# Kernel optimization log

Hardware: AMD Instinct MI355X
Metric: run time of the kernel (lower is better)

## Reference

```python
import jax, jax.numpy as jnp
import numpy as np

B, T, C, H, K = 4, 2048, 1024, 16, 64
CHUNK = 64
NUM_LAYERS, LAYER_ID = 12, 6
D_MIX, D_DECAY = 32, 64


def setup_inputs() -> dict:
    key = jax.random.key(0)
    ks = jax.random.split(key, 12)
    x = jax.random.normal(ks[0], (B, T, C), jnp.float32)
    shift_state_in = jax.random.normal(ks[1], (B, C), jnp.float32)
    wkv_state_in = jnp.zeros((B, H, K, K), jnp.float32)

    r01 = LAYER_ID / max(NUM_LAYERS - 1, 1)
    r10 = 1.0 - LAYER_ID / NUM_LAYERS
    ddd = (np.arange(C, dtype=np.float64) / C)
    maa = lambda p: jnp.asarray((1.0 - ddd ** p).reshape(1, 1, C), jnp.float32)
    time_maa_x = maa(r10)
    time_maa_w = maa(r10)
    time_maa_k = maa(r10)
    time_maa_v = jnp.asarray((1.0 - (ddd ** r10 + 0.3 * r01)).reshape(1, 1, C), jnp.float32)
    time_maa_r = maa(0.5 * r10)
    time_maa_g = maa(0.5 * r10)
    time_maa_w1 = jax.random.uniform(ks[2], (C, D_MIX * 5), jnp.float32, -0.01, 0.01)
    time_maa_w2 = jax.random.uniform(ks[3], (5, D_MIX, C), jnp.float32, -0.01, 0.01)

    n = np.arange(C, dtype=np.float64)
    time_decay = jnp.asarray((-6 + 5 * (n / (C - 1)) ** (0.7 + 1.3 * r01)).reshape(1, 1, C), jnp.float32)
    time_decay_w1 = jax.random.uniform(ks[4], (C, D_DECAY), jnp.float32, -0.01, 0.01)
    time_decay_w2 = jax.random.uniform(ks[5], (D_DECAY, C), jnp.float32, -0.01, 0.01)

    zig = ((n + 1) % 3 - 1) * 0.1
    time_faaaa = jnp.asarray((r01 * (1 - n / (C - 1)) + zig).reshape(H, K), jnp.float32)
    lucid_temperature = jnp.ones((1, H, 1, 1), jnp.float32)

    s = 0.02
    W_r = jax.random.normal(ks[6], (C, C), jnp.float32) * s
    W_k = jax.random.normal(ks[7], (C, C), jnp.float32) * s
    W_v = jax.random.normal(ks[8], (C, C), jnp.float32) * s
    W_g = jax.random.normal(ks[9], (C, C), jnp.float32) * s
    W_o = jax.random.normal(ks[10], (C, C), jnp.float32) * s
    ln_gamma = jnp.ones((C,), jnp.float32)
    ln_beta = jnp.zeros((C,), jnp.float32)

    return dict(x=x, shift_state_in=shift_state_in, wkv_state_in=wkv_state_in,
                time_maa_x=time_maa_x, time_maa_w=time_maa_w, time_maa_k=time_maa_k,
                time_maa_v=time_maa_v, time_maa_r=time_maa_r, time_maa_g=time_maa_g,
                time_maa_w1=time_maa_w1, time_maa_w2=time_maa_w2,
                time_decay=time_decay, time_decay_w1=time_decay_w1, time_decay_w2=time_decay_w2,
                time_faaaa=time_faaaa, lucid_temperature=lucid_temperature,
                W_r=W_r, W_k=W_k, W_v=W_v, W_g=W_g, W_o=W_o,
                ln_gamma=ln_gamma, ln_beta=ln_beta)


def _forward(x, shift_state_in, wkv_state_in, time_maa_x, time_maa_w, time_maa_k,
             time_maa_v, time_maa_r, time_maa_g, time_maa_w1, time_maa_w2,
             time_decay, time_decay_w1, time_decay_w2, time_faaaa, lucid_temperature,
             W_r, W_k, W_v, W_g, W_o, ln_gamma, ln_beta):
    # ddlerp token shift
    dxprev = jnp.concatenate([shift_state_in[:, None, :], x[:, :-1]], axis=1) - x
    xxx = jnp.tanh((x + dxprev * time_maa_x) @ time_maa_w1).reshape(B, T, 5, D_MIX)
    m = jnp.einsum('btfd,fdc->fbtc', xxx, time_maa_w2)  # (5,B,T,C)
    mw, mk, mv, mr, mg = m[0], m[1], m[2], m[3], m[4]
    xw = x + dxprev * (time_maa_w + mw)
    xk = x + dxprev * (time_maa_k + mk)
    xv = x + dxprev * (time_maa_v + mv)
    xr = x + dxprev * (time_maa_r + mr)
    xg = x + dxprev * (time_maa_g + mg)

    r = xr @ W_r.T
    k = xk @ W_k.T
    v = xv @ W_v.T
    g = jax.nn.silu(xg @ W_g.T)
    w = time_decay + jnp.tanh(xw @ time_decay_w1) @ time_decay_w2

    tohead = lambda a: a.reshape(B, T, H, K).transpose(0, 2, 1, 3)  # (B,H,T,K)
    r_h, k_h, v_h = tohead(r), tohead(k), tohead(v)
    w_h = -jnp.exp(tohead(w))  # log-decay, negative
    u = time_faaaa.reshape(1, H, 1, K)
    temp = jax.nn.softplus(lucid_temperature)  # (1,H,1,1)

    n_chunks = T // CHUNK
    tochunks = lambda a: a.reshape(B, H, n_chunks, CHUNK, K).transpose(2, 0, 1, 3, 4)
    eye = jnp.eye(CHUNK, dtype=jnp.float32)
    mid = CHUNK // 2

    def step(state, inp):
        r_c, k_c, v_c, w_log = inp  # each (B,H,cs,K)
        w_cum = jnp.cumsum(w_log, axis=-2)
        w_shift = jnp.pad(w_cum[..., :-1, :], ((0, 0), (0, 0), (1, 0), (0, 0)))
        offset = w_shift[..., mid:mid + 1, :]
        r_decay = jnp.exp(jnp.clip(w_shift - offset, -30, 30))
        k_inv_decay = jnp.exp(jnp.clip(offset - w_cum, -30, 30))
        A = jnp.einsum('bhtk,bhsk->bhts', r_c * r_decay, k_c * k_inv_decay)
        A = jnp.tril(A, -1) + eye * jnp.sum(r_c * (u * k_c), axis=-1)[..., None]
        k_norm = k_c / jnp.maximum(jnp.linalg.norm(k_c, axis=-1, keepdims=True), 1e-12)
        K_gram = jnp.einsum('bhtk,bhsk->bhts', k_norm, k_norm)
        P = eye + jnp.exp(jnp.clip(temp * K_gram, -20, 20))
        P_v = jnp.linalg.solve(P, v_c)
        w_intra = jnp.exp(jnp.clip(w_cum - w_log, -30, 30))
        y = A @ P_v + (r_c * w_intra) @ state
        w_sum = jnp.sum(w_log, axis=-2, keepdims=True)  # (B,H,1,K)
        w_inter = jnp.exp(jnp.clip(w_sum - w_cum, -30, 30))
        new_state = state * jnp.exp(w_sum) + jnp.einsum('bhtk,bhtv->bhkv', k_c * w_inter, v_c)
        return new_state, y

    state_out, ys = jax.lax.scan(
        step, wkv_state_in,
        (tochunks(r_h), tochunks(k_h), tochunks(v_h), tochunks(w_h)))
    # (n,B,H,cs,K) -> (B,T,C)
    y = ys.transpose(1, 2, 0, 3, 4).reshape(B, H, T, K).transpose(0, 2, 1, 3).reshape(B, T, C)

    # GroupNorm with n_head groups, eps = 1e-5 * head_size_divisor**2
    eps = 1e-5 * 64.0
    yg = y.reshape(B, T, H, K)
    mu = yg.mean(axis=-1, keepdims=True)
    var = yg.var(axis=-1, keepdims=True)
    yn = (yg - mu) / jnp.sqrt(var + eps)
    yn = yn * ln_gamma.reshape(1, 1, H, K) + ln_beta.reshape(1, 1, H, K)
    yn = yn.reshape(B, T, C)

    out = (yn * g) @ W_o.T
    return out, x[:, -1], state_out


def reference(x, shift_state_in, wkv_state_in, time_maa_x, time_maa_w, time_maa_k,
              time_maa_v, time_maa_r, time_maa_g, time_maa_w1, time_maa_w2,
              time_decay, time_decay_w1, time_decay_w2, time_faaaa, lucid_temperature,
              W_r, W_k, W_v, W_g, W_o, ln_gamma, ln_beta):
    return _forward(x, shift_state_in, wkv_state_in, time_maa_x, time_maa_w, time_maa_k,
                    time_maa_v, time_maa_r, time_maa_g, time_maa_w1, time_maa_w2,
                    time_decay, time_decay_w1, time_decay_w2, time_faaaa, lucid_temperature,
                    W_r, W_k, W_v, W_g, W_o, ln_gamma, ln_beta)
```

## Files before the change

kernel.cpp:

```cpp
#include <hip/hip_runtime.h>
#include <cstdint>
#include <cstddef>

typedef unsigned short ushort_t;
#define DEVI __device__ __forceinline__

constexpr int Bc = 4, Tc = 2048, Cc = 1024, Hc = 16;
constexpr int BT = Bc * Tc;
constexpr int NCHUNK = Tc / 64;

using f32x4  = __attribute__((ext_vector_type(4))) float;
using bf16x8 = __attribute__((ext_vector_type(8))) __bf16;

DEVI ushort_t f2bf(float f) {
  union { float f; unsigned u; } v; v.f = f;
  unsigned r = v.u + 0x7fffu + ((v.u >> 16) & 1u);
  return (ushort_t)(r >> 16);
}
DEVI float bf2f(ushort_t u) {
  union { unsigned u; float f; } v; v.u = ((unsigned)u) << 16; return v.f;
}
DEVI float clip30(float x) { return fminf(fmaxf(x, -30.f), 30.f); }
DEVI float clip20(float x) { return fminf(fmaxf(x, -20.f), 20.f); }

DEVI float4 bf4up(uint2 r) {
  float4 v;
  v.x = bf2f((ushort_t)(r.x & 0xffff)); v.y = bf2f((ushort_t)(r.x >> 16));
  v.z = bf2f((ushort_t)(r.y & 0xffff)); v.w = bf2f((ushort_t)(r.y >> 16));
  return v;
}
DEVI uint2 f4pk(float4 v) {
  uint2 r;
  r.x = (unsigned)f2bf(v.x) | ((unsigned)f2bf(v.y) << 16);
  r.y = (unsigned)f2bf(v.z) | ((unsigned)f2bf(v.w) << 16);
  return r;
}

DEVI void gload_lds16(const ushort_t* g, ushort_t* l) {
  __builtin_amdgcn_global_load_lds(
      (const __attribute__((address_space(1))) void*)g,
      (__attribute__((address_space(3))) void*)l, 16, 0, 0);
}

#define GETEL(V4, E) ((E) == 0 ? (V4).x : (E) == 1 ? (V4).y : (E) == 2 ? (V4).z : (V4).w)
#define SETEL(V4, E, VAL) do { if ((E) == 0) (V4).x = (VAL); else if ((E) == 1) (V4).y = (VAL); \
                               else if ((E) == 2) (V4).z = (VAL); else (V4).w = (VAL); } while (0)

__global__ void k_f2bf5(const float* __restrict__ i0, const float* __restrict__ i1,
                        const float* __restrict__ i2, const float* __restrict__ i3,
                        const float* __restrict__ i4,
                        ushort_t* __restrict__ o0, ushort_t* __restrict__ o1,
                        ushort_t* __restrict__ o2, ushort_t* __restrict__ o3,
                        ushort_t* __restrict__ o4) {
  int z = blockIdx.z;
  const float* in = (z == 0) ? i0 : (z == 1) ? i1 : (z == 2) ? i2 : (z == 3) ? i3 : i4;
  ushort_t* out   = (z == 0) ? o0 : (z == 1) ? o1 : (z == 2) ? o2 : (z == 3) ? o3 : o4;
  int i = blockIdx.x * 256 + threadIdx.x;
  if (i < Cc * Cc / 4) {
    float4 v = *(const float4*)(in + (size_t)i * 4);
    ushort4 o;
    o.x = f2bf(v.x); o.y = f2bf(v.y); o.z = f2bf(v.z); o.w = f2bf(v.w);
    *(ushort4*)(out + (size_t)i * 4) = o;
  }
}

__global__ void k_prep(const float* __restrict__ w2, const float* __restrict__ w1,
                       const float* __restrict__ dw1, const float* __restrict__ x,
                       ushort_t* __restrict__ w2t, ushort_t* __restrict__ w1t,
                       ushort_t* __restrict__ dw1t, float* __restrict__ xlast) {
  int i = blockIdx.x * 256 + threadIdx.x;
  if (i < 163840) {
    int c = i / 160, fd = i % 160;
    w2t[i] = f2bf(w2[(size_t)fd * 1024 + c]);
  } else if (i < 327680) {
    int j = i - 163840; int n = j >> 10, r = j & 1023;
    w1t[j] = f2bf(w1[(size_t)r * 160 + n]);
  } else if (i < 393216) {
    int j = i - 327680; int n = j >> 10, r = j & 1023;
    dw1t[j] = f2bf(dw1[(size_t)r * 64 + n]);
  } else if (i < 397312) {
    int j = i - 393216; int b = j >> 10, c = j & 1023;
    xlast[j] = x[((size_t)b * Tc + Tc - 1) * Cc + c];
  }
}

__global__ __launch_bounds__(256) void k_shift_tanh(
    const float* __restrict__ x, const float* __restrict__ sst,
    const float* __restrict__ tmx, const ushort_t* __restrict__ Wt,
    ushort_t* __restrict__ outv) {
  constexpr int NCOLS = 160, NF = NCOLS / 16;
  int tid = threadIdx.x;
  int wave = tid >> 6, lane = tid & 63;
  int row0 = (blockIdx.x * 4 + wave) * 16;
  int lr = lane & 15, lk = (lane >> 4) * 8;
  int rg = row0 + lr;
  int tt = rg & (Tc - 1);
  const float* xrow = x + (size_t)rg * Cc;
  const float* prow = (tt == 0) ? (sst + (size_t)(rg >> 11) * Cc) : (xrow - Cc);
  f32x4 acc[NF];
  #pragma unroll
  for (int n = 0; n < NF; ++n) acc[n] = (f32x4){0.f, 0.f, 0.f, 0.f};
  for (int k0 = 0; k0 < 1024; k0 += 32) {
    int c0 = k0 + lk;
    float4 xa = *(const float4*)(xrow + c0), xb = *(const float4*)(xrow + c0 + 4);
    float4 pa = *(const float4*)(prow + c0), pb = *(const float4*)(prow + c0 + 4);
    float4 ta = *(const float4*)(tmx + c0), tb = *(const float4*)(tmx + c0 + 4);
    union { bf16x8 v; uint2 u[2]; } cv;
    cv.u[0] = f4pk(make_float4(xa.x + (pa.x - xa.x) * ta.x, xa.y + (pa.y - xa.y) * ta.y,
                               xa.z + (pa.z - xa.z) * ta.z, xa.w + (pa.w - xa.w) * ta.w));
    cv.u[1] = f4pk(make_float4(xb.x + (pb.x - xb.x) * tb.x, xb.y + (pb.y - xb.y) * tb.y,
                               xb.z + (pb.z - xb.z) * tb.z, xb.w + (pb.w - xb.w) * tb.w));
    #pragma unroll
    for (int n = 0; n < NF; ++n) {
      bf16x8 b = *(const bf16x8*)&Wt[(size_t)(n * 16 + lr) * 1024 + k0 + lk];
      acc[n] = __builtin_amdgcn_mfma_f32_16x16x32_bf16(cv.v, b, acc[n], 0, 0, 0);
    }
  }
  #pragma unroll
  for (int n = 0; n < NF; ++n) {
    #pragma unroll
    for (int q = 0; q < 4; ++q) {
      int row = row0 + (lane >> 4) * 4 + q;
      size_t oi = (size_t)row * NCOLS + n * 16 + lr;
      outv[oi] = f2bf(tanhf(acc[n][q]));
    }
  }
}

template<int NCOLS, int OBF>
__global__ __launch_bounds__(256) void k_tanh_mfma(const ushort_t* __restrict__ A,
                                                   const ushort_t* __restrict__ Wt,
                                                   void* __restrict__ outv) {
  constexpr int NF = NCOLS / 16;
  int tid = threadIdx.x;
  int wave = tid >> 6, lane = tid & 63;
  int row0 = (blockIdx.x * 4 + wave) * 16;
  int lr = lane & 15, lk = (lane >> 4) * 8;
  f32x4 acc[NF];
  #pragma unroll
  for (int n = 0; n < NF; ++n) acc[n] = (f32x4){0.f, 0.f, 0.f, 0.f};
  for (int k0 = 0; k0 < 1024; k0 += 32) {
    bf16x8 a = *(const bf16x8*)&A[(size_t)(row0 + lr) * 1024 + k0 + lk];
    #pragma unroll
    for (int n = 0; n < NF; ++n) {
      bf16x8 b = *(const bf16x8*)&Wt[(size_t)(n * 16 + lr) * 1024 + k0 + lk];
      acc[n] = __builtin_amdgcn_mfma_f32_16x16x32_bf16(a, b, acc[n], 0, 0, 0);
    }
  }
  #pragma unroll
  for (int n = 0; n < NF; ++n) {
    #pragma unroll
    for (int q = 0; q < 4; ++q) {
      int row = row0 + (lane >> 4) * 4 + q;
      size_t oi = (size_t)row * NCOLS + n * 16 + lr;
      float v = tanhf(acc[n][q]);
      if (OBF == 1) ((ushort_t*)outv)[oi] = f2bf(v);
      else          ((float*)outv)[oi] = v;
    }
  }
}

__global__ __launch_bounds__(256) void k_mix5m(
    const float* __restrict__ x, const float* __restrict__ sst,
    const ushort_t* __restrict__ t160b, const ushort_t* __restrict__ w2t,
    const float* __restrict__ maaw, const float* __restrict__ maak,
    const float* __restrict__ maav, const float* __restrict__ maar,
    const float* __restrict__ maag,
    ushort_t* __restrict__ xw, ushort_t* __restrict__ xk, ushort_t* __restrict__ xv,
    ushort_t* __restrict__ xr, ushort_t* __restrict__ xg) {
  __shared__ __align__(16) ushort_t smem[23040];
  ushort_t* As = smem;
  ushort_t* Bs = smem + 64 * 168;
  ushort_t* sT = smem;
  int tid = threadIdx.x;
  int lane = tid & 63;
  int bRow = blockIdx.x * 64, bCol = blockIdx.y * 64;
  #pragma unroll
  for (int i = 0; i < 5; ++i) {
    int e = tid + i * 256;
    int r = e / 20, cc = (e % 20) * 8;
    *(int4*)&As[r * 168 + cc] = *(const int4*)&t160b[(size_t)(bRow + r) * 160 + cc];
    *(int4*)&Bs[r * 168 + cc] = *(const int4*)&w2t[(size_t)(bCol + r) * 160 + cc];
  }
  __syncthreads();
  int wm = tid >> 7, wn = (tid >> 6) & 1;
  f32x4 acc[5][2][2];
  #pragma unroll
  for (int f = 0; f < 5; ++f)
    #pragma unroll
    for (int m = 0; m < 2; ++m)
      #pragma unroll
      for (int n = 0; n < 2; ++n) acc[f][m][n] = (f32x4){0.f, 0.f, 0.f, 0.f};
  #pragma unroll
  for (int f = 0; f < 5; ++f) {
    bf16x8 af[2], bfv[2];
    #pragma unroll
    for (int m = 0; m < 2; ++m)
      af[m] = *(const bf16x8*)&As[(wm * 32 + m * 16 + (lane & 15)) * 168 + f * 32 + (lane >> 4) * 8];
    #pragma unroll
    for (int n = 0; n < 2; ++n)
      bfv[n] = *(const bf16x8*)&Bs[(wn * 32 + n * 16 + (lane & 15)) * 168 + f * 32 + (lane >> 4) * 8];
    #pragma unroll
    for (int m = 0; m < 2; ++m)
      #pragma unroll
      for (int n = 0; n < 2; ++n)
        acc[f][m][n] = __builtin_amdgcn_mfma_f32_16x16x32_bf16(af[m], bfv[n], acc[f][m][n], 0, 0, 0);
  }
  __syncthreads();
  #pragma unroll
  for (int n = 0; n < 2; ++n) {
    int colL = wn * 32 + n * 16 + (lane & 15);
    int col = bCol + colL;
    float mw_c = maaw[col], mk_c = maak[col], mv_c = maav[col];
    float mr_c = maar[col], mg_c = maag[col];
    #pragma unroll
    for (int m = 0; m < 2; ++m) {
      int rowL0 = wm * 32 + m * 16 + (lane >> 4) * 4;
      #pragma unroll
      for (int q = 0; q < 4; ++q) {
        int rL = rowL0 + q;
        int rg = bRow + rL;
        int tt = rg & (Tc - 1);
        size_t g = (size_t)rg * Cc + col;
        float xv0 = x[g];
        float xprev = (tt == 0) ? sst[(size_t)(rg >> 11) * Cc + col] : x[g - Cc];
        float dv = xprev - xv0;
        sT[0 * 4608 + rL * 72 + colL] = f2bf(xv0 + dv * (mw_c + acc[0][m][n][q]));
        sT[1 * 4608 + rL * 72 + colL] = f2bf(xv0 + dv * (mk_c + acc[1][m][n][q]));
        sT[2 * 4608 + rL * 72 + colL] = f2bf(xv0 + dv * (mv_c + acc[2][m][n][q]));
        sT[3 * 4608 + rL * 72 + colL] = f2bf(xv0 + dv * (mr_c + acc[3][m][n][q]));
        sT[4 * 4608 + rL * 72 + colL] = f2bf(xv0 + dv * (mg_c + acc[4][m][n][q]));
      }
    }
  }
  __syncthreads();
  #pragma unroll
  for (int f = 0; f < 5; ++f) {
    ushort_t* dst = (f == 0) ? xw : (f == 1) ? xk : (f == 2) ? xv : (f == 3) ? xr : xg;
    #pragma unroll
    for (int j = 0; j < 2; ++j) {
      int e = tid + j * 256;
      int r = e >> 3, ch = (e & 7) * 8;
      *(int4*)&dst[(size_t)(bRow + r) * 1024 + bCol + ch] =
          *(const int4*)&sT[f * 4608 + r * 72 + ch];
    }
  }
}

template<int EPI, int OBF>
DEVI void gemm_body(const ushort_t* __restrict__ A, const ushort_t* __restrict__ Wt,
                    void* __restrict__ outv, ushort_t* As, ushort_t* Bs,
                    int bRow, int bCol) {
  int tid = threadIdx.x;
  int wave = tid >> 6, lane = tid & 63;
  int wm = wave >> 1, wn = wave & 1;
  int lr = lane >> 2;
  int lkb = (((lane & 3) ^ ((lane >> 3) & 3))) * 8;
  int pch = ((lane >> 4) ^ ((lane >> 1) & 3)) * 8;
  f32x4 zero4 = {0.f, 0.f, 0.f, 0.f};
  f32x4 acc[4][4];
  #pragma unroll
  for (int m = 0; m < 4; ++m)
    #pragma unroll
    for (int n = 0; n < 4; ++n) acc[m][n] = zero4;

#define STAGEK(OFS, K0) do { \
    _Pragma("unroll") \
    for (int i = 0; i < 2; ++i) { \
      int row = (wave + 4 * i) * 16 + lr; \
      gload_lds16(A + (size_t)(bRow + row) * 1024 + (K0) + lkb, &As[(OFS) + (wave + 4 * i) * 512]); \
      gload_lds16(Wt + (size_t)(bCol + row) * 1024 + (K0) + lkb, &Bs[(OFS) + (wave + 4 * i) * 512]); \
    } } while (0)
#define CMP(OFS) do { \
    bf16x8 af[4], bfv[4]; \
    _Pragma("unroll") \
    for (int m = 0; m < 4; ++m) \
      af[m] = *(const bf16x8*)&As[(OFS) + (wm * 64 + m * 16 + (lane & 15)) * 32 + pch]; \
    _Pragma("unroll") \
    for (int n = 0; n < 4; ++n) \
      bfv[n] = *(const bf16x8*)&Bs[(OFS) + (wn * 64 + n * 16 + (lane & 15)) * 32 + pch]; \
    _Pragma("unroll") \
    for (int m = 0; m < 4; ++m) \
      _Pragma("unroll") \
      for (int n = 0; n < 4; ++n) \
        acc[m][n] = __builtin_amdgcn_mfma_f32_16x16x32_bf16(af[m], bfv[n], acc[m][n], 0, 0, 0); \
  } while (0)

  for (int k0 = 0; k0 < 1024; k0 += 64) {
    STAGEK(0, k0);
    STAGEK(4096, k0 + 32);
    __syncthreads();
    CMP(0);
    CMP(4096);
    __syncthreads();
  }
#undef STAGEK
#undef CMP

  #pragma unroll
  for (int m = 0; m < 4; ++m) {
    int row = bRow + wm * 64 + m * 16 + (lane >> 4) * 4;
    #pragma unroll
    for (int n = 0; n < 4; ++n) {
      int col = bCol + wn * 64 + n * 16 + (lane & 15);
      #pragma unroll
      for (int q = 0; q < 4; ++q) {
        float v = acc[m][n][q];
        if (EPI == 1) v = v / (1.f + __expf(-v));
        size_t oi = (size_t)(row + q) * 1024 + col;
        if (OBF == 1) ((ushort_t*)outv)[oi] = f2bf(v);
        else          ((float*)outv)[oi] = v;
      }
    }
  }
}

__global__ __launch_bounds__(256) void k_gemm4(
    const ushort_t* __restrict__ A0, const ushort_t* __restrict__ A1,
    const ushort_t* __restrict__ A2, const ushort_t* __restrict__ A3,
    const ushort_t* __restrict__ W0, const ushort_t* __restrict__ W1,
    const ushort_t* __restrict__ W2, const ushort_t* __restrict__ W3,
    ushort_t* __restrict__ O0, ushort_t* __restrict__ O1,
    ushort_t* __restrict__ O2, ushort_t* __restrict__ O3) {
  __shared__ __align__(16) ushort_t As[2 * 128 * 32];
  __shared__ __align__(16) ushort_t Bs[2 * 128 * 32];
  int z = blockIdx.z;
  const ushort_t* A  = (z == 0) ? A0 : (z == 1) ? A1 : (z == 2) ? A2 : A3;
  const ushort_t* Wt = (z == 0) ? W0 : (z == 1) ? W1 : (z == 2) ? W2 : W3;
  ushort_t* out      = (z == 0) ? O0 : (z == 1) ? O1 : (z == 2) ? O2 : O3;
  if (z == 3) gemm_body<1, 1>(A, Wt, out, As, Bs, blockIdx.x * 128, blockIdx.y * 128);
  else        gemm_body<0, 1>(A, Wt, out, As, Bs, blockIdx.x * 128, blockIdx.y * 128);
}

__global__ __launch_bounds__(256) void k_gemm_bm64(const ushort_t* __restrict__ A,
                                                   const ushort_t* __restrict__ Wt,
                                                   float* __restrict__ out) {
  __shared__ __align__(16) ushort_t As[2 * 64 * 32];
  __shared__ __align__(16) ushort_t Bs[2 * 128 * 32];
  int tid = threadIdx.x;
  int wave = tid >> 6, lane = tid & 63;
  int lr = lane >> 2;
  int lkb = (((lane & 3) ^ ((lane >> 3) & 3))) * 8;
  int pch = ((lane >> 4) ^ ((lane >> 1) & 3)) * 8;
  int bRow = blockIdx.x * 64, bCol = blockIdx.y * 128;
  f32x4 acc[4][2];
  #pragma unroll
  for (int m = 0; m < 4; ++m)
    #pragma unroll
    for (int n = 0; n < 2; ++n) acc[m][n] = (f32x4){0.f, 0.f, 0.f, 0.f};

#define STAGEK64(OA, OB, K0) do { \
    { int row = wave * 16 + lr; \
      gload_lds16(A + (size_t)(bRow + row) * 1024 + (K0) + lkb, &As[(OA) + wave * 512]); } \
    _Pragma("unroll") \
    for (int i = 0; i < 2; ++i) { \
      int row = (wave + 4 * i) * 16 + lr; \
      gload_lds16(Wt + (size_t)(bCol + row) * 1024 + (K0) + lkb, &Bs[(OB) + (wave + 4 * i) * 512]); \
    } } while (0)
#define CMP64(OA, OB) do { \
    bf16x8 af[4], bfv[2]; \
    _Pragma("unroll") \
    for (int m = 0; m < 4; ++m) \
      af[m] = *(const bf16x8*)&As[(OA) + (m * 16 + (lane & 15)) * 32 + pch]; \
    _Pragma("unroll") \
    for (int n = 0; n < 2; ++n) \
      bfv[n] = *(const bf16x8*)&Bs[(OB) + (wave * 32 + n * 16 + (lane & 15)) * 32 + pch]; \
    _Pragma("unroll") \
    for (int m = 0; m < 4; ++m) \
      _Pragma("unroll") \
      for (int n = 0; n < 2; ++n) \
        acc[m][n] = __builtin_amdgcn_mfma_f32_16x16x32_bf16(af[m], bfv[n], acc[m][n], 0, 0, 0); \
  } while (0)

  for (int k0 = 0; k0 < 1024; k0 += 64) {
    STAGEK64(0, 0, k0);
    STAGEK64(2048, 4096, k0 + 32);
    __syncthreads();
    CMP64(0, 0);
    CMP64(2048, 4096);
    __syncthreads();
  }
#undef STAGEK64
#undef CMP64

  #pragma unroll
  for (int m = 0; m < 4; ++m) {
    int row = bRow + m * 16 + (lane >> 4) * 4;
    #pragma unroll
    for (int n = 0; n < 2; ++n) {
      int col = bCol + wave * 32 + n * 16 + (lane & 15);
      #pragma unroll
      for (int q = 0; q < 4; ++q)
        out[(size_t)(row + q) * 1024 + col] = acc[m][n][q];
    }
  }
}

__global__ __launch_bounds__(256) void k_preA(
    const ushort_t* __restrict__ rbuf, const ushort_t* __restrict__ kbuf,
    const ushort_t* __restrict__ vbf,
    const ushort_t* __restrict__ t64bf, const float* __restrict__ dw2,
    const float* __restrict__ tdec, const float* __restrict__ faaaa,
    ushort_t* __restrict__ rwbf, ushort_t* __restrict__ kvbf, ushort_t* __restrict__ knbuf,
    ushort_t* __restrict__ Abf, float* __restrict__ esum) {
  __shared__ __align__(16) char ubuf[16640 + 9216 + 9216];
  float* wc = (float*)ubuf;
  ushort_t* sS = (ushort_t*)ubuf;
  ushort_t* sA = (ushort_t*)(ubuf + 16640);
  ushort_t* sB = (ushort_t*)(ubuf + 16640 + 9216);
  __shared__ float sred[4 * 64];
  __shared__ float sdiag[64];
  __shared__ float snrm[64];
  int bx = blockIdx.x;
  int ci = bx & 31, bh = bx >> 5;
  int b = bh >> 4, h = bh & 15;
  int tid = threadIdx.x;
  int w = tid >> 6, lane = tid & 63;
  int c = lane;
  int row0g = b * Tc + ci * 64;
  size_t base = (size_t)row0g * Cc + (size_t)h * 64;

  #pragma unroll
  for (int j = 0; j < 2; ++j) {
    int e = tid + j * 256; int r = e >> 3, cc = (e & 7) * 8;
    *(int4*)&sA[r * 72 + cc] = *(const int4*)&t64bf[(size_t)(row0g + r) * 64 + cc];
  }
  for (int i = 0; i < 16; ++i) {
    int e = tid + i * 256; int r = e >> 6, cc = e & 63;
    sB[cc * 72 + r] = f2bf(dw2[(size_t)r * Cc + h * 64 + cc]);
  }
  float rv[16], kv[16];
  #pragma unroll
  for (int i = 0; i < 16; ++i) {
    size_t g = base + (size_t)(w * 16 + i) * Cc + c;
    rv[i] = bf2f(rbuf[g]); kv[i] = bf2f(kbuf[g]);
  }
  __syncthreads();
  {
    int rbase = w * 16;
    bf16x8 a0 = *(const bf16x8*)&sA[(rbase + (lane & 15)) * 72 + (lane >> 4) * 8];
    bf16x8 a1 = *(const bf16x8*)&sA[(rbase + (lane & 15)) * 72 + 32 + (lane >> 4) * 8];
    #pragma unroll
    for (int ct = 0; ct < 4; ++ct) {
      bf16x8 b0 = *(const bf16x8*)&sB[(ct * 16 + (lane & 15)) * 72 + (lane >> 4) * 8];
      bf16x8 b1 = *(const bf16x8*)&sB[(ct * 16 + (lane & 15)) * 72 + 32 + (lane >> 4) * 8];
      f32x4 acc = {0.f, 0.f, 0.f, 0.f};
      acc = __builtin_amdgcn_mfma_f32_16x16x32_bf16(a0, b0, acc, 0, 0, 0);
      acc = __builtin_amdgcn_mfma_f32_16x16x32_bf16(a1, b1, acc, 0, 0, 0);
      int s = ct * 16 + (lane & 15);
      #pragma unroll
      for (int q = 0; q < 4; ++q) {
        int t = rbase + (lane >> 4) * 4 + q;
        wc[t * 65 + s] = acc[q];
      }
    }
  }
  __syncthreads();
  float wv[16];
  {
    float td = tdec[h * 64 + c];
    #pragma unroll
    for (int i = 0; i < 16; ++i)
      wv[i] = -__expf(td + wc[(w * 16 + i) * 65 + c]);
  }
  {
    float s = 0.f;
    #pragma unroll
    for (int i = 0; i < 16; ++i) s += wv[i];
    sred[w * 64 + c] = s;
  }
  __syncthreads();
  {
    float run = 0.f;
    for (int ww = 0; ww < w; ++ww) run += sred[ww * 64 + c];
    #pragma unroll
    for (int i = 0; i < 16; ++i) {
      run += wv[i]; wv[i] = run;
      wc[(w * 16 + i) * 65 + c] = run;
    }
    if (w == 3) esum[((size_t)bh * 32 + ci) * 64 + c] = __expf(run);
  }
  {
    float u_c = faaaa[h * 64 + c];
    #pragma unroll
    for (int i = 0; i < 16; ++i) {
      float p = rv[i] * kv[i] * u_c;
      float n2 = kv[i] * kv[i];
      #pragma unroll
      for (int o = 32; o; o >>= 1) { p += __shfl_xor(p, o, 64); n2 += __shfl_xor(n2, o, 64); }
      if (lane == 0) {
        sdiag[w * 16 + i] = p;
        snrm[w * 16 + i] = 1.f / fmaxf(sqrtf(n2), 1e-12f);
      }
    }
  }
  __syncthreads();
  float off32 = wc[31 * 65 + c];
  float wc63 = wc[63 * 65 + c];
  #pragma unroll
  for (int i = 0; i < 16; ++i) {
    int t = w * 16 + i;
    size_t g = base + (size_t)t * Cc + c;
    float wsh = (i == 0) ? ((w == 0) ? 0.f : wc[(t - 1) * 65 + c]) : wv[i - 1];
    rwbf[g] = f2bf(rv[i] * __expf(clip30(wsh)));
    sA[t * 72 + c] = f2bf(rv[i] * __expf(clip30(wsh - off32)));
    sB[t * 72 + c] = f2bf(kv[i] * __expf(clip30(off32 - wv[i])));
    knbuf[g] = f2bf(kv[i] * snrm[t]);
  }
  __syncthreads();
  {
    int rbase = w * 16;
    bf16x8 a0 = *(const bf16x8*)&sA[(rbase + (lane & 15)) * 72 + (lane >> 4) * 8];
    bf16x8 a1 = *(const bf16x8*)&sA[(rbase + (lane & 15)) * 72 + 32 + (lane >> 4) * 8];
    #pragma unroll
    for (int ct = 0; ct < 4; ++ct) {
      bf16x8 b0 = *(const bf16x8*)&sB[(ct * 16 + (lane & 15)) * 72 + (lane >> 4) * 8];
      bf16x8 b1 = *(const bf16x8*)&sB[(ct * 16 + (lane & 15)) * 72 + 32 + (lane >> 4) * 8];
      f32x4 acc = {0.f, 0.f, 0.f, 0.f};
      acc = __builtin_amdgcn_mfma_f32_16x16x32_bf16(a0, b0, acc, 0, 0, 0);
      acc = __builtin_amdgcn_mfma_f32_16x16x32_bf16(a1, b1, acc, 0, 0, 0);
      int s = ct * 16 + (lane & 15);
      #pragma unroll
      for (int q = 0; q < 4; ++q) {
        int t = rbase + (lane >> 4) * 4 + q;
        float val = (t > s) ? acc[q] : ((t == s) ? sdiag[t] : 0.f);
        sS[t * 72 + s] = f2bf(val);
      }
    }
  }
  __syncthreads();
  #pragma unroll
  for (int j = 0; j < 2; ++j) {
    int e = tid + j * 256;
    int r = e >> 3, ch = (e & 7) * 8;
    *(int4*)&Abf[(size_t)bx * 4096 + r * 64 + ch] = *(const int4*)&sS[r * 72 + ch];
  }
  #pragma unroll
  for (int i = 0; i < 16; ++i) {
    int t = w * 16 + i;
    sA[c * 72 + t] = f2bf(kv[i] * __expf(clip30(wc63 - wv[i])));
    sB[c * 72 + t] = vbf[base + (size_t)t * Cc + c];
  }
  __syncthreads();
  {
    int rbase = w * 16;
    bf16x8 a0 = *(const bf16x8*)&sA[(rbase + (lane & 15)) * 72 + (lane >> 4) * 8];
    bf16x8 a1 = *(const bf16x8*)&sA[(rbase + (lane & 15)) * 72 + 32 + (lane >> 4) * 8];
    #pragma unroll
    for (int ct = 0; ct < 4; ++ct) {
      bf16x8 b0 = *(const bf16x8*)&sB[(ct * 16 + (lane & 15)) * 72 + (lane >> 4) * 8];
      bf16x8 b1 = *(const bf16x8*)&sB[(ct * 16 + (lane & 15)) * 72 + 32 + (lane >> 4) * 8];
      f32x4 acc = {0.f, 0.f, 0.f, 0.f};
      acc = __builtin_amdgcn_mfma_f32_16x16x32_bf16(a0, b0, acc, 0, 0, 0);
      acc = __builtin_amdgcn_mfma_f32_16x16x32_bf16(a1, b1, acc, 0, 0, 0);
      int j = ct * 16 + (lane & 15);
      #pragma unroll
      for (int q = 0; q < 4; ++q) {
        int ii = rbase + (lane >> 4) * 4 + q;
        sS[ii * 72 + j] = f2bf(acc[q]);
      }
    }
  }
  __syncthreads();
  #pragma unroll
  for (int j = 0; j < 2; ++j) {
    int e = tid + j * 256;
    int r = e >> 3, ch = (e & 7) * 8;
    *(int4*)&kvbf[base + (size_t)r * Cc + ch] = *(const int4*)&sS[r * 72 + ch];
  }
}

__global__ __launch_bounds__(256) void k_preB(
    const ushort_t* __restrict__ knbuf, const ushort_t* __restrict__ vbf,
    const ushort_t* __restrict__ Abf, const ushort_t* __restrict__ rwbf,
    const ushort_t* __restrict__ statebuf, const float* __restrict__ ltemp,
    const ushort_t* __restrict__ gbuf, const float* __restrict__ gamma,
    const float* __restrict__ beta, ushort_t* __restrict__ ong) {
  __shared__ __align__(16) ushort_t sKX[64 * 72];
  __shared__ __align__(16) ushort_t sAb[64 * 72];
  __shared__ __align__(16) char ubuf[64 * 72 * 2 * 2];
  __shared__ __align__(16) float pivbuf[2][192];
  __shared__ float colbuf[2][64];
  __shared__ float diagbuf[64];
  float* sP = (float*)ubuf;
  ushort_t* sRW = (ushort_t*)ubuf;
  ushort_t* sSTt = (ushort_t*)(ubuf + 64 * 72 * 2);

  int bx = blockIdx.x;
  int ci = bx & 31, bh = bx >> 5;
  int b = bh >> 4, h = bh & 15;
  int tid = threadIdx.x;
  int w = tid >> 6, lane = tid & 63;
  int rg = tid >> 4, cg = tid & 15;
  size_t base = ((size_t)(b * Tc + ci * 64)) * Cc + (size_t)h * 64;

  #pragma unroll
  for (int j = 0; j < 2; ++j) {
    int e = tid + j * 256;
    int r = e >> 3, cc = (e & 7) * 8;
    *(int4*)&sKX[r * 72 + cc] = *(const int4*)&knbuf[base + (size_t)r * Cc + cc];
    *(int4*)&sAb[r * 72 + cc] = *(const int4*)&Abf[(size_t)bx * 4096 + (size_t)r * 64 + cc];
  }
  float4 A0, A1, A2, A3, B0, B1, B2, B3;
  if (cg >= 8) {
#define LDV(R, AR, BR) do { \
      int4 raw = *(const int4*)(vbf + base + (size_t)(4 * rg + (R)) * Cc + (cg - 8) * 8); \
      (AR).x = bf2f((ushort_t)(raw.x & 0xffff)); (AR).y = bf2f((ushort_t)((unsigned)raw.x >> 16)); \
      (AR).z = bf2f((ushort_t)(raw.y & 0xffff)); (AR).w = bf2f((ushort_t)((unsigned)raw.y >> 16)); \
      (BR).x = bf2f((ushort_t)(raw.z & 0xffff)); (BR).y = bf2f((ushort_t)((unsigned)raw.z >> 16)); \
      (BR).z = bf2f((ushort_t)(raw.w & 0xffff)); (BR).w = bf2f((ushort_t)((unsigned)raw.w >> 16)); \
    } while (0)
    LDV(0, A0, B0); LDV(1, A1, B1); LDV(2, A2, B2); LDV(3, A3, B3);
#undef LDV
  }
  __syncthreads();
  float temp = log1pf(__expf(ltemp[h]));
  {
    int rbase = w * 16;
    bf16x8 a0 = *(const bf16x8*)&sKX[(rbase + (lane & 15)) * 72 + (lane >> 4) * 8];
    bf16x8 a1 = *(const bf16x8*)&sKX[(rbase + (lane & 15)) * 72 + 32 + (lane >> 4) * 8];
    #pragma unroll
    for (int ct = 0; ct < 4; ++ct) {
      bf16x8 b0 = *(const bf16x8*)&sKX[(ct * 16 + (lane & 15)) * 72 + (lane >> 4) * 8];
      bf16x8 b1 = *(const bf16x8*)&sKX[(ct * 16 + (lane & 15)) * 72 + 32 + (lane >> 4) * 8];
      f32x4 acc = {0.f, 0.f, 0.f, 0.f};
      acc = __builtin_amdgcn_mfma_f32_16x16x32_bf16(a0, b0, acc, 0, 0, 0);
      acc = __builtin_amdgcn_mfma_f32_16x16x32_bf16(a1, b1, acc, 0, 0, 0);
      int s = ct * 16 + (lane & 15);
      #pragma unroll
      for (int q = 0; q < 4; ++q) {
        int t = rbase + (lane >> 4) * 4 + q;
        sP[t * 68 + s] = ((t == s) ? 1.f : 0.f) + __expf(clip20(temp * acc[q]));
      }
    }
  }
  __syncthreads();
  if (cg < 8) {
    A0 = *(float4*)&sP[(4 * rg + 0) * 68 + cg * 8]; B0 = *(float4*)&sP[(4 * rg + 0) * 68 + cg * 8 + 4];
    A1 = *(float4*)&sP[(4 * rg + 1) * 68 + cg * 8]; B1 = *(float4*)&sP[(4 * rg + 1) * 68 + cg * 8 + 4];
    A2 = *(float4*)&sP[(4 * rg + 2) * 68 + cg * 8]; B2 = *(float4*)&sP[(4 * rg + 2) * 68 + cg * 8 + 4];
    A3 = *(float4*)&sP[(4 * rg + 3) * 68 + cg * 8]; B3 = *(float4*)&sP[(4 * rg + 3) * 68 + cg * 8 + 4];
  }
  __syncthreads();
  #pragma unroll
  for (int j = 0; j < 2; ++j) {
    int e = tid + j * 256;
    int r = e >> 3, cc = (e & 7) * 8;
    *(int4*)&sRW[r * 72 + cc] = *(const int4*)&rwbf[base + (size_t)r * Cc + cc];
  }
  {
    const ushort_t* sb = statebuf + ((size_t)bh * 32 + ci) * 4096;
    #pragma unroll
    for (int i = 0; i < 16; ++i) {
      int e = tid + i * 256;
      int r = e >> 6, c = e & 63;
      sSTt[c * 72 + r] = sb[e];
    }
  }
#define UPD(MA, MB, F) do { \
    (MA).x -= (F) * p0_.x; (MA).y -= (F) * p0_.y; (MA).z -= (F) * p0_.z; (MA).w -= (F) * p0_.w; \
    (MB).x -= (F) * p1_.x; (MB).y -= (F) * p1_.y; (MB).z -= (F) * p1_.z; (MB).w -= (F) * p1_.w; \
  } while (0)
#define GJSTEP(JL, PRA, PRB, H0, H1, H2, H3) do { \
    int j_ = jh * 8 + (JL); \
    if (rg == (j_ >> 2)) { \
      *(float4*)&pivbuf[(JL) & 1][cg * 12]     = (PRA); \
      *(float4*)&pivbuf[(JL) & 1][cg * 12 + 4] = (PRB); \
    } \
    if (cg == jh) { \
      float4 cv_; \
      cv_.x = GETEL(H0, (JL) & 3); \
      cv_.y = GETEL(H1, (JL) & 3); \
      cv_.z = GETEL(H2, (JL) & 3); \
      cv_.w = GETEL(H3, (JL) & 3); \
      *(float4*)&colbuf[(JL) & 1][rg * 4] = cv_; \
    } \
    __syncthreads(); \
    float pd_ = pivbuf[(JL) & 1][(j_ >> 3) * 12 + (j_ & 7)]; \
    float4 fv_ = *(float4*)&colbuf[(JL) & 1][rg * 4]; \
    float4 p0_ = *(float4*)&pivbuf[(JL) & 1][cg * 12]; \
    float4 p1_ = *(float4*)&pivbuf[(JL) & 1][cg * 12 + 4]; \
    if (rg == (j_ >> 2)) SETEL(fv_, (JL) & 3, 0.f); \
    float inv_ = 1.f / pd_; \
    float f0_ = fv_.x * inv_, f1_ = fv_.y * inv_, f2_ = fv_.z * inv_, f3_ = fv_.w * inv_; \
    UPD(A0, B0, f0_); UPD(A1, B1, f1_); UPD(A2, B2, f2_); UPD(A3, B3, f3_); \
  } while (0)
  for (int jh = 0; jh < 8; ++jh) {
    GJSTEP(0, A0, B0, A0, A1, A2, A3);
    GJSTEP(1, A1, B1, A0, A1, A2, A3);
    GJSTEP(2, A2, B2, A0, A1, A2, A3);
    GJSTEP(3, A3, B3, A0, A1, A2, A3);
    GJSTEP(4, A0, B0, B0, B1, B2, B3);
    GJSTEP(5, A1, B1, B0, B1, B2, B3);
    GJSTEP(6, A2, B2, B0, B1, B2, B3);
    GJSTEP(7, A3, B3, B0, B1, B2, B3);
  }
#undef GJSTEP
#undef UPD
  if (cg == (rg >> 1)) {
    float4 h0 = (rg & 1) ? B0 : A0;
    float4 h1 = (rg & 1) ? B1 : A1;
    float4 h2 = (rg & 1) ? B2 : A2;
    float4 h3 = (rg & 1) ? B3 : A3;
    *(float4*)&diagbuf[rg * 4] = make_float4(h0.x, h1.y, h2.z, h3.w);
  }
  __syncthreads();
  if (cg >= 8) {
    float4 dg = *(float4*)&diagbuf[rg * 4];
#define WRX(R, AR, BR, IR) do { \
      int cb_ = (cg - 8) * 8; \
      sKX[(cb_ + 0) * 72 + 4 * rg + (R)] = f2bf((AR).x * (IR)); \
      sKX[(cb_ + 1) * 72 + 4 * rg + (R)] = f2bf((AR).y * (IR)); \
      sKX[(cb_ + 2) * 72 + 4 * rg + (R)] = f2bf((AR).z * (IR)); \
      sKX[(cb_ + 3) * 72 + 4 * rg + (R)] = f2bf((AR).w * (IR)); \
      sKX[(cb_ + 4) * 72 + 4 * rg + (R)] = f2bf((BR).x * (IR)); \
      sKX[(cb_ + 5) * 72 + 4 * rg + (R)] = f2bf((BR).y * (IR)); \
      sKX[(cb_ + 6) * 72 + 4 * rg + (R)] = f2bf((BR).z * (IR)); \
      sKX[(cb_ + 7) * 72 + 4 * rg + (R)] = f2bf((BR).w * (IR)); \
    } while (0)
    WRX(0, A0, B0, 1.f / dg.x);
    WRX(1, A1, B1, 1.f / dg.y);
    WRX(2, A2, B2, 1.f / dg.z);
    WRX(3, A3, B3, 1.f / dg.w);
#undef WRX
  }
  __syncthreads();
  {
    int rbase = w * 16;
    bf16x8 aA0 = *(const bf16x8*)&sAb[(rbase + (lane & 15)) * 72 + (lane >> 4) * 8];
    bf16x8 aA1 = *(const bf16x8*)&sAb[(rbase + (lane & 15)) * 72 + 32 + (lane >> 4) * 8];
    bf16x8 aR0 = *(const bf16x8*)&sRW[(rbase + (lane & 15)) * 72 + (lane >> 4) * 8];
    bf16x8 aR1 = *(const bf16x8*)&sRW[(rbase + (lane & 15)) * 72 + 32 + (lane >> 4) * 8];
    f32x4 yv[4];
    #pragma unroll
    for (int ct = 0; ct < 4; ++ct) {
      bf16x8 bX0 = *(const bf16x8*)&sKX[(ct * 16 + (lane & 15)) * 72 + (lane >> 4) * 8];
      bf16x8 bX1 = *(const bf16x8*)&sKX[(ct * 16 + (lane & 15)) * 72 + 32 + (lane >> 4) * 8];
      bf16x8 bS0 = *(const bf16x8*)&sSTt[(ct * 16 + (lane & 15)) * 72 + (lane >> 4) * 8];
      bf16x8 bS1 = *(const bf16x8*)&sSTt[(ct * 16 + (lane & 15)) * 72 + 32 + (lane >> 4) * 8];
      f32x4 acc = {0.f, 0.f, 0.f, 0.f};
      acc = __builtin_amdgcn_mfma_f32_16x16x32_bf16(aA0, bX0, acc, 0, 0, 0);
      acc = __builtin_amdgcn_mfma_f32_16x16x32_bf16(aA1, bX1, acc, 0, 0, 0);
      acc = __builtin_amdgcn_mfma_f32_16x16x32_bf16(aR0, bS0, acc, 0, 0, 0);
      acc = __builtin_amdgcn_mfma_f32_16x16x32_bf16(aR1, bS1, acc, 0, 0, 0);
      yv[ct] = acc;
    }
    #pragma unroll
    for (int q = 0; q < 4; ++q) {
      float s1 = yv[0][q] + yv[1][q] + yv[2][q] + yv[3][q];
      float s2 = yv[0][q] * yv[0][q] + yv[1][q] * yv[1][q] +
                 yv[2][q] * yv[2][q] + yv[3][q] * yv[3][q];
      #pragma unroll
      for (int o = 1; o < 16; o <<= 1) {
        s1 += __shfl_xor(s1, o, 64);
        s2 += __shfl_xor(s2, o, 64);
      }
      float mu = s1 * (1.f / 64.f);
      float var = s2 * (1.f / 64.f) - mu * mu;
      float rs = rsqrtf(var + 6.4e-4f);
      int t = rbase + (lane >> 4) * 4 + q;
      #pragma unroll
      for (int ct = 0; ct < 4; ++ct) {
        int cc = ct * 16 + (lane & 15);
        size_t g = base + (size_t)t * Cc + cc;
        float yn = (yv[ct][q] - mu) * rs;
        float o = (yn * gamma[h * 64 + cc] + beta[h * 64 + cc]) * bf2f(gbuf[g]);
        sAb[t * 72 + cc] = f2bf(o);
      }
    }
  }
  __syncthreads();
  #pragma unroll
  for (int j = 0; j < 2; ++j) {
    int e = tid + j * 256;
    int r = e >> 3, ch = (e & 7) * 8;
    *(int4*)&ong[base + (size_t)r * Cc + ch] = *(const int4*)&sAb[r * 72 + ch];
  }
}

__global__ __launch_bounds__(128) void k_scanstate(
    const float* __restrict__ wkv0, const ushort_t* __restrict__ kvbf,
    const float* __restrict__ esum, ushort_t* __restrict__ statebuf,
    float* __restrict__ stout) {
  int bh = blockIdx.x >> 3;
  int rg = blockIdx.x & 7;
  int b = bh >> 4, h = bh & 15;
  int tid = threadIdx.x;
  int r = rg * 8 + (tid >> 4);
  int c0 = (tid & 15) * 4;
  float4 st = *(const float4*)(wkv0 + ((size_t)bh * 64 + r) * 64 + c0);
  size_t kvb = (size_t)(b * Tc) * Cc + (size_t)h * 64 + (size_t)r * Cc + c0;
  constexpr int PF = 4;
  uint2 kvn[PF];
  float4 evn[PF];
  #pragma unroll
  for (int j = 0; j < PF; ++j) {
    kvn[j] = *(const uint2*)(kvbf + kvb + (size_t)j * 64 * Cc);
    evn[j] = *(const float4*)(esum + ((size_t)bh * 32 + j) * 64 + c0);
  }
  #pragma unroll
  for (int ci = 0; ci < NCHUNK; ++ci) {
    *(uint2*)(statebuf + ((size_t)bh * 32 + ci) * 4096 + (size_t)r * 64 + c0) = f4pk(st);
    float4 kv = bf4up(kvn[ci & 3]);
    float4 ev = evn[ci & 3];
    if (ci + PF < NCHUNK) {
      kvn[ci & 3] = *(const uint2*)(kvbf + kvb + (size_t)(ci + PF) * 64 * Cc);
      evn[ci & 3] = *(const float4*)(esum + ((size_t)bh * 32 + ci + PF) * 64 + c0);
    }
    st.x = st.x * ev.x + kv.x;
    st.y = st.y * ev.y + kv.y;
    st.z = st.z * ev.z + kv.z;
    st.w = st.w * ev.w + kv.w;
  }
  *(float4*)(stout + ((size_t)bh * 64 + r) * 64 + c0) = st;
}

extern "C" void kernel_launch(void* const* d_in, const int* in_sizes, int n_in,
                              void* d_out, int out_size, void* d_ws, size_t ws_size,
                              hipStream_t stream) {
  (void)in_sizes; (void)n_in; (void)out_size;
  const float* x     = (const float*)d_in[0];
  const float* sst   = (const float*)d_in[1];
  const float* wkv0  = (const float*)d_in[2];
  const float* tmx   = (const float*)d_in[3];
  const float* tmw   = (const float*)d_in[4];
  const float* tmk   = (const float*)d_in[5];
  const float* tmv   = (const float*)d_in[6];
  const float* tmr   = (const float*)d_in[7];
  const float* tmg   = (const float*)d_in[8];
  const float* w1    = (const float*)d_in[9];
  const float* w2    = (const float*)d_in[10];
  const float* tdec  = (const float*)d_in[11];
  const float* dw1   = (const float*)d_in[12];
  const float* dw2   = (const float*)d_in[13];
  const float* faaaa = (const float*)d_in[14];
  const float* ltemp = (const float*)d_in[15];
  const float* Wr    = (const float*)d_in[16];
  const float* Wk    = (const float*)d_in[17];
  const float* Wv    = (const float*)d_in[18];
  const float* Wg    = (const float*)d_in[19];
  const float* Wo    = (const float*)d_in[20];
  const float* lng   = (const float*)d_in[21];
  const float* lnb   = (const float*)d_in[22];
  float* out = (float*)d_out;

  const size_t MB = 1ull << 20;
  const size_t NEED = 242 * MB;
  if (ws_size < NEED) return;

  char* p = (char*)d_ws;
  ushort_t* kbb  = (ushort_t*)(p + 0 * MB);
  ushort_t* xwb  = (ushort_t*)(p + 16 * MB);
  ushort_t* rbb  = (ushort_t*)(p + 16 * MB);
  ushort_t* kvbf = (ushort_t*)(p + 32 * MB);
  ushort_t* statebuf = (ushort_t*)(p + 96 * MB);
  ushort_t* vbuf = (ushort_t*)(p + 128 * MB);
  ushort_t* gbuf = (ushort_t*)(p + 144 * MB);
  ushort_t* xkb  = (ushort_t*)(p + 160 * MB);
  ushort_t* Abf  = (ushort_t*)(p + 160 * MB);
  ushort_t* xvb  = (ushort_t*)(p + 176 * MB);
  ushort_t* rwbf = (ushort_t*)(p + 176 * MB);
  ushort_t* xrb  = (ushort_t*)(p + 192 * MB);
  ushort_t* xgb  = (ushort_t*)(p + 208 * MB);
  ushort_t* t160b = (ushort_t*)(p + 224 * MB);
  float*    esum = (float*)(p + 224 * MB);
  ushort_t* w2t  = (ushort_t*)(p + 227 * MB);
  ushort_t* w1t  = (ushort_t*)(p + 228 * MB);
  ushort_t* dw1t = (ushort_t*)(p + 229 * MB);
  ushort_t* t64bf = (ushort_t*)(p + 230 * MB);
  ushort_t* Wrb  = (ushort_t*)(p + 232 * MB);
  ushort_t* Wkb  = (ushort_t*)(p + 234 * MB);
  ushort_t* Wvb  = (ushort_t*)(p + 236 * MB);
  ushort_t* Wgb  = (ushort_t*)(p + 238 * MB);
  ushort_t* Wob  = (ushort_t*)(p + 240 * MB);

  const int thr = 256;
  k_f2bf5<<<dim3((Cc * Cc / 4 + 255) / 256, 1, 5), thr, 0, stream>>>(
      Wr, Wk, Wv, Wg, Wo, Wrb, Wkb, Wvb, Wgb, Wob);
  k_prep<<<(397312 + 255) / 256, thr, 0, stream>>>(w2, w1, dw1, x,
                                                   w2t, w1t, dw1t, out + (size_t)BT * Cc);

  k_shift_tanh<<<BT / 64, thr, 0, stream>>>(x, sst, tmx, w1t, t160b);
  k_mix5m<<<dim3(BT / 64, Cc / 64), thr, 0, stream>>>(x, sst, t160b, w2t,
                                                      tmw, tmk, tmv, tmr, tmg,
                                                      xwb, xkb, xvb, xrb, xgb);
  k_tanh_mfma<64, 1><<<BT / 64, thr, 0, stream>>>(xwb, dw1t, t64bf);

  k_gemm4<<<dim3(BT / 128, Cc / 128, 4), thr, 0, stream>>>(
      xrb, xkb, xvb, xgb, Wrb, Wkb, Wvb, Wgb, rbb, kbb, vbuf, gbuf);

  k_preA<<<2048, thr, 0, stream>>>(rbb, kbb, vbuf, t64bf, dw2, tdec, faaaa,
                                   rwbf, kvbf, xgb , Abf, esum);
  k_scanstate<<<512, 128, 0, stream>>>(wkv0, kvbf, esum, statebuf,
                                       out + (size_t)BT * Cc + (size_t)Bc * Cc);
  k_preB<<<2048, thr, 0, stream>>>(xgb , vbuf, Abf, rwbf, statebuf, ltemp,
                                   gbuf, lng, lnb, xgb );

  k_gemm_bm64<<<dim3(BT / 64, Cc / 128), thr, 0, stream>>>(xgb, Wob, out);
}
```

Measured before the change: 390.7 us.

## Merge prep kernels, fold decay tanh GEMM into gemm batch, stage output stores

Merges the weight-conversion and prep kernels into one launch with a sixth z-slice. Folds the 64-column tanh projection into the 4-way projection GEMM launch as a fifth z-slice, so it runs alongside the big GEMMs instead of as a separate serialized launch. The final output GEMM now stages its tile through shared memory and writes coalesced float4 rows. The r buffer moves to a separate workspace region so it no longer aliases xw, which the concurrently running tanh slice still reads.

```diff
diff --git a/kernel.cpp b/kernel.cpp
--- a/kernel.cpp
+++ b/kernel.cpp
@@ -46,41 +46,41 @@
 #define SETEL(V4, E, VAL) do { if ((E) == 0) (V4).x = (VAL); else if ((E) == 1) (V4).y = (VAL); \
                                else if ((E) == 2) (V4).z = (VAL); else (V4).w = (VAL); } while (0)
 
-__global__ void k_f2bf5(const float* __restrict__ i0, const float* __restrict__ i1,
-                        const float* __restrict__ i2, const float* __restrict__ i3,
-                        const float* __restrict__ i4,
-                        ushort_t* __restrict__ o0, ushort_t* __restrict__ o1,
-                        ushort_t* __restrict__ o2, ushort_t* __restrict__ o3,
-                        ushort_t* __restrict__ o4) {
+__global__ void k_f2bf5p(const float* __restrict__ i0, const float* __restrict__ i1,
+                         const float* __restrict__ i2, const float* __restrict__ i3,
+                         const float* __restrict__ i4,
+                         const float* __restrict__ w2, const float* __restrict__ w1,
+                         const float* __restrict__ dw1, const float* __restrict__ x,
+                         ushort_t* __restrict__ o0, ushort_t* __restrict__ o1,
+                         ushort_t* __restrict__ o2, ushort_t* __restrict__ o3,
+                         ushort_t* __restrict__ o4,
+                         ushort_t* __restrict__ w2t, ushort_t* __restrict__ w1t,
+                         ushort_t* __restrict__ dw1t, float* __restrict__ xlast) {
   int z = blockIdx.z;
+  int i = blockIdx.x * 256 + threadIdx.x;
+  if (z == 5) {
+    if (i < 163840) {
+      int c = i / 160, fd = i % 160;
+      w2t[i] = f2bf(w2[(size_t)fd * 1024 + c]);
+    } else if (i < 327680) {
+      int j = i - 163840; int n = j >> 10, r = j & 1023;
+      w1t[j] = f2bf(w1[(size_t)r * 160 + n]);
+    } else if (i < 393216) {
+      int j = i - 327680; int n = j >> 10, r = j & 1023;
+      dw1t[j] = f2bf(dw1[(size_t)r * 64 + n]);
+    } else if (i < 397312) {
+      int j = i - 393216; int b = j >> 10, c = j & 1023;
+      xlast[j] = x[((size_t)b * Tc + Tc - 1) * Cc + c];
+    }
+    return;
+  }
   const float* in = (z == 0) ? i0 : (z == 1) ? i1 : (z == 2) ? i2 : (z == 3) ? i3 : i4;
   ushort_t* out   = (z == 0) ? o0 : (z == 1) ? o1 : (z == 2) ? o2 : (z == 3) ? o3 : o4;
-  int i = blockIdx.x * 256 + threadIdx.x;
   if (i < Cc * Cc / 4) {
     float4 v = *(const float4*)(in + (size_t)i * 4);
     ushort4 o;
     o.x = f2bf(v.x); o.y = f2bf(v.y); o.z = f2bf(v.z); o.w = f2bf(v.w);
     *(ushort4*)(out + (size_t)i * 4) = o;
-  }
-}
-
-__global__ void k_prep(const float* __restrict__ w2, const float* __restrict__ w1,
-                       const float* __restrict__ dw1, const float* __restrict__ x,
-                       ushort_t* __restrict__ w2t, ushort_t* __restrict__ w1t,
-                       ushort_t* __restrict__ dw1t, float* __restrict__ xlast) {
-  int i = blockIdx.x * 256 + threadIdx.x;
-  if (i < 163840) {
-    int c = i / 160, fd = i % 160;
-    w2t[i] = f2bf(w2[(size_t)fd * 1024 + c]);
-  } else if (i < 327680) {
-    int j = i - 163840; int n = j >> 10, r = j & 1023;
-    w1t[j] = f2bf(w1[(size_t)r * 160 + n]);
-  } else if (i < 393216) {
-    int j = i - 327680; int n = j >> 10, r = j & 1023;
-    dw1t[j] = f2bf(dw1[(size_t)r * 64 + n]);
-  } else if (i < 397312) {
-    int j = i - 393216; int b = j >> 10, c = j & 1023;
-    xlast[j] = x[((size_t)b * Tc + Tc - 1) * Cc + c];
   }
 }
 
@@ -127,14 +127,12 @@
   }
 }
 
-template<int NCOLS, int OBF>
-__global__ __launch_bounds__(256) void k_tanh_mfma(const ushort_t* __restrict__ A,
-                                                   const ushort_t* __restrict__ Wt,
-                                                   void* __restrict__ outv) {
-  constexpr int NF = NCOLS / 16;
+DEVI void tanh64_body(const ushort_t* __restrict__ A, const ushort_t* __restrict__ Wt,
+                      ushort_t* __restrict__ outv, int bid) {
+  constexpr int NF = 4;
   int tid = threadIdx.x;
   int wave = tid >> 6, lane = tid & 63;
-  int row0 = (blockIdx.x * 4 + wave) * 16;
+  int row0 = (bid * 4 + wave) * 16;
   int lr = lane & 15, lk = (lane >> 4) * 8;
   f32x4 acc[NF];
   #pragma unroll
@@ -152,10 +150,7 @@
     #pragma unroll
     for (int q = 0; q < 4; ++q) {
       int row = row0 + (lane >> 4) * 4 + q;
-      size_t oi = (size_t)row * NCOLS + n * 16 + lr;
-      float v = tanhf(acc[n][q]);
-      if (OBF == 1) ((ushort_t*)outv)[oi] = f2bf(v);
-      else          ((float*)outv)[oi] = v;
+      outv[(size_t)row * 64 + n * 16 + lr] = f2bf(tanhf(acc[n][q]));
     }
   }
 }
@@ -315,16 +310,23 @@
   }
 }
 
-__global__ __launch_bounds__(256) void k_gemm4(
+__global__ __launch_bounds__(256) void k_gemm5(
     const ushort_t* __restrict__ A0, const ushort_t* __restrict__ A1,
     const ushort_t* __restrict__ A2, const ushort_t* __restrict__ A3,
     const ushort_t* __restrict__ W0, const ushort_t* __restrict__ W1,
     const ushort_t* __restrict__ W2, const ushort_t* __restrict__ W3,
     ushort_t* __restrict__ O0, ushort_t* __restrict__ O1,
-    ushort_t* __restrict__ O2, ushort_t* __restrict__ O3) {
+    ushort_t* __restrict__ O2, ushort_t* __restrict__ O3,
+    const ushort_t* __restrict__ xwb, const ushort_t* __restrict__ dw1t,
+    ushort_t* __restrict__ t64bf) {
+  int z = blockIdx.z;
+  if (z == 4) {
+    int bid = blockIdx.y * 64 + blockIdx.x;
+    if (bid < BT / 64) tanh64_body(xwb, dw1t, t64bf, bid);
+    return;
+  }
   __shared__ __align__(16) ushort_t As[2 * 128 * 32];
   __shared__ __align__(16) ushort_t Bs[2 * 128 * 32];
-  int z = blockIdx.z;
   const ushort_t* A  = (z == 0) ? A0 : (z == 1) ? A1 : (z == 2) ? A2 : A3;
   const ushort_t* Wt = (z == 0) ? W0 : (z == 1) ? W1 : (z == 2) ? W2 : W3;
   ushort_t* out      = (z == 0) ? O0 : (z == 1) ? O1 : (z == 2) ? O2 : O3;
@@ -335,8 +337,10 @@
 __global__ __launch_bounds__(256) void k_gemm_bm64(const ushort_t* __restrict__ A,
                                                    const ushort_t* __restrict__ Wt,
                                                    float* __restrict__ out) {
-  __shared__ __align__(16) ushort_t As[2 * 64 * 32];
-  __shared__ __align__(16) ushort_t Bs[2 * 128 * 32];
+  __shared__ __align__(16) char ub[64 * 132 * 4];
+  ushort_t* As = (ushort_t*)ub;
+  ushort_t* Bs = (ushort_t*)(ub + 8192);
+  float* sT = (float*)ub;
   int tid = threadIdx.x;
   int wave = tid >> 6, lane = tid & 63;
   int lr = lane >> 2;
@@ -385,14 +389,21 @@
 
   #pragma unroll
   for (int m = 0; m < 4; ++m) {
-    int row = bRow + m * 16 + (lane >> 4) * 4;
+    int rL = m * 16 + (lane >> 4) * 4;
     #pragma unroll
     for (int n = 0; n < 2; ++n) {
-      int col = bCol + wave * 32 + n * 16 + (lane & 15);
+      int cL = wave * 32 + n * 16 + (lane & 15);
       #pragma unroll
       for (int q = 0; q < 4; ++q)
-        out[(size_t)(row + q) * 1024 + col] = acc[m][n][q];
-    }
+        sT[(rL + q) * 132 + cL] = acc[m][n][q];
+    }
+  }
+  __syncthreads();
+  #pragma unroll
+  for (int j = 0; j < 8; ++j) {
+    int e = tid + j * 256;
+    int r = e >> 5, c4 = (e & 31) * 4;
+    *(float4*)&out[(size_t)(bRow + r) * 1024 + bCol + c4] = *(const float4*)&sT[r * 132 + c4];
   }
 }
 
@@ -851,7 +862,7 @@
   char* p = (char*)d_ws;
   ushort_t* kbb  = (ushort_t*)(p + 0 * MB);
   ushort_t* xwb  = (ushort_t*)(p + 16 * MB);
-  ushort_t* rbb  = (ushort_t*)(p + 16 * MB);
+  ushort_t* rbb  = (ushort_t*)(p + 48 * MB);
   ushort_t* kvbf = (ushort_t*)(p + 32 * MB);
   ushort_t* statebuf = (ushort_t*)(p + 96 * MB);
   ushort_t* vbuf = (ushort_t*)(p + 128 * MB);
@@ -875,19 +886,18 @@
   ushort_t* Wob  = (ushort_t*)(p + 240 * MB);
 
   const int thr = 256;
-  k_f2bf5<<<dim3((Cc * Cc / 4 + 255) / 256, 1, 5), thr, 0, stream>>>(
-      Wr, Wk, Wv, Wg, Wo, Wrb, Wkb, Wvb, Wgb, Wob);
-  k_prep<<<(397312 + 255) / 256, thr, 0, stream>>>(w2, w1, dw1, x,
-                                                   w2t, w1t, dw1t, out + (size_t)BT * Cc);
+  k_f2bf5p<<<dim3(1552, 1, 6), thr, 0, stream>>>(
+      Wr, Wk, Wv, Wg, Wo, w2, w1, dw1, x,
+      Wrb, Wkb, Wvb, Wgb, Wob, w2t, w1t, dw1t, out + (size_t)BT * Cc);
 
   k_shift_tanh<<<BT / 64, thr, 0, stream>>>(x, sst, tmx, w1t, t160b);
   k_mix5m<<<dim3(BT / 64, Cc / 64), thr, 0, stream>>>(x, sst, t160b, w2t,
                                                       tmw, tmk, tmv, tmr, tmg,
                                                       xwb, xkb, xvb, xrb, xgb);
-  k_tanh_mfma<64, 1><<<BT / 64, thr, 0, stream>>>(xwb, dw1t, t64bf);
-
-  k_gemm4<<<dim3(BT / 128, Cc / 128, 4), thr, 0, stream>>>(
-      xrb, xkb, xvb, xgb, Wrb, Wkb, Wvb, Wgb, rbb, kbb, vbuf, gbuf);
+
+  k_gemm5<<<dim3(BT / 128, Cc / 128, 5), thr, 0, stream>>>(
+      xrb, xkb, xvb, xgb, Wrb, Wkb, Wvb, Wgb, rbb, kbb, vbuf, gbuf,
+      xwb, dw1t, t64bf);
 
   k_preA<<<2048, thr, 0, stream>>>(rbb, kbb, vbuf, t64bf, dw2, tdec, faaaa,
                                    rwbf, kvbf, xgb , Abf, esum);
```

Result: no change. 384.5 us (-1.6%).
